# Performance work log

Measured on AMD Instinct MI355X. Metric: run time of the kernel, lower is better.

## Reference

```python
import jax, jax.numpy as jnp
import numpy as np

HIDDEN = 2048
NUM_EXPERTS = 64
TOP_K = 2


def setup_inputs() -> dict:
    key = jax.random.key(0)
    k1, k2 = jax.random.split(key)
    x = jax.random.normal(k1, (4, 4096, HIDDEN), dtype=jnp.float32)
    # nn.Linear(hidden, num_experts, bias=False): weight shape [E, H], y = x @ W.T
    W = jax.random.normal(k2, (NUM_EXPERTS, HIDDEN), dtype=jnp.float32) * (HIDDEN ** -0.5)
    return {"x": x, "W": W}


def reference(x, W):
    B, S, H = x.shape
    E, K = NUM_EXPERTS, TOP_K
    xf = x.reshape(-1, H)                       # [N, H]
    gate_logits = xf @ W.T                      # [N, E]
    routing_probs = jax.nn.softmax(gate_logits, axis=-1)
    top_k_probs, top_k_indices = jax.lax.top_k(routing_probs, K)  # [N, K]
    denom = jnp.sum(top_k_probs, axis=-1, keepdims=True) + 1e-6
    routing_weights = (top_k_probs / denom).reshape(B, S, K)
    expert_indices = top_k_indices.reshape(B, S, K)

    # aux load-balancing loss (training path)
    N = xf.shape[0]
    # expert_mask.mean(0): fraction of tokens assigned to each expert
    assign_per_expert = jnp.zeros((E,), jnp.float32).at[top_k_indices.reshape(-1)].add(1.0) / N
    prob_per_expert = jnp.mean(routing_probs, axis=0)             # [E]
    aux_loss = (jnp.sum(prob_per_expert * prob_per_expert) * E
                + jnp.sum(assign_per_expert * assign_per_expert) * E)

    # expert_counts update (bincount over selected indices)
    expert_counts = jnp.zeros((E,), jnp.float32).at[top_k_indices.reshape(-1)].add(1.0)

    return routing_weights, expert_indices, aux_loss, expert_counts
```

## Files before the change

kernel.cpp:

```cpp
#include <hip/hip_runtime.h>

#define HID 2048
#define NEXP 64
#define NTOK 16384
#define TM 32
#define NTHREADS 512
#define NCHUNK 32
#define KPH 8
#define CPW 4
#define TPW 4
#define WS_W_OFF 1024
#define CHUNK_B 24576

#define OUT_IDX_OFF (2 * NTOK)
#define OUT_AUX_OFF (4 * NTOK)
#define OUT_CNT_OFF (4 * NTOK + 1)

typedef __attribute__((ext_vector_type(8))) short bhalf8;
typedef __attribute__((ext_vector_type(16))) float f32x16;

__device__ __forceinline__ void split3(float v, unsigned short& h1, unsigned short& h2, unsigned short& h3) {
    unsigned int u = __float_as_uint(v);
    unsigned int r1 = (u + 0x7FFFu + ((u >> 16) & 1u)) & 0xFFFF0000u;
    float f1 = __uint_as_float(r1);
    float d1 = v - f1;
    unsigned int u2 = __float_as_uint(d1);
    unsigned int r2 = (u2 + 0x7FFFu + ((u2 >> 16) & 1u)) & 0xFFFF0000u;
    float f2 = __uint_as_float(r2);
    float d2 = d1 - f2;
    h1 = (unsigned short)(r1 >> 16);
    h2 = (unsigned short)(r2 >> 16);
    h3 = (unsigned short)(__float_as_uint(d2) >> 16);
}

__device__ __forceinline__ void xsplit(float4 va, float4 vb, bhalf8& o1, bhalf8& o2, bhalf8& o3) {
    float f[8] = {va.x, va.y, va.z, va.w, vb.x, vb.y, vb.z, vb.w};
    union U { bhalf8 v; unsigned int u[4]; } u1, u2, u3;
#pragma unroll
    for (int t = 0; t < 4; t++) {
        float a = f[2 * t], b = f[2 * t + 1];
        unsigned int ua = __float_as_uint(a), ub = __float_as_uint(b);
        float da = a - __uint_as_float(ua & 0xFFFF0000u);
        float db = b - __uint_as_float(ub & 0xFFFF0000u);
        unsigned int uda = __float_as_uint(da), udb = __float_as_uint(db);
        float da2 = da - __uint_as_float(uda & 0xFFFF0000u);
        float db2 = db - __uint_as_float(udb & 0xFFFF0000u);
        u1.u[t] = (ua >> 16) | (ub & 0xFFFF0000u);
        u2.u[t] = (uda >> 16) | (udb & 0xFFFF0000u);
        u3.u[t] = (__float_as_uint(da2) >> 16) | (__float_as_uint(db2) & 0xFFFF0000u);
    }
    o1 = u1.v; o2 = u2.v; o3 = u3.v;
}

__global__ __launch_bounds__(64) void wsplit_kernel(const float* __restrict__ W,
                                                    char* __restrict__ wq,
                                                    float* __restrict__ wsf) {
    if (blockIdx.x < 2) wsf[blockIdx.x * 64 + threadIdx.x] = 0.f;
    int idx8 = (blockIdx.x * 64 + threadIdx.x) * 8;
    int e = idx8 >> 11;
    int k0 = idx8 & 2047;
    int c = k0 >> 6, ks = (k0 >> 4) & 3, half = (k0 >> 3) & 1;
    int g = e >> 5, l = (e & 31) + 32 * half;
    const float4* wp = (const float4*)(W + (size_t)e * HID + k0);
    float4 v0 = wp[0], v1 = wp[1];
    float f[8] = {v0.x, v0.y, v0.z, v0.w, v1.x, v1.y, v1.z, v1.w};
    unsigned int p1[4], p2[4], p3[4];
#pragma unroll
    for (int t = 0; t < 4; t++) {
        unsigned short a1, a2, a3, b1, b2, b3;
        split3(f[2 * t], a1, a2, a3);
        split3(f[2 * t + 1], b1, b2, b3);
        p1[t] = (unsigned int)a1 | ((unsigned int)b1 << 16);
        p2[t] = (unsigned int)a2 | ((unsigned int)b2 << 16);
        p3[t] = (unsigned int)a3 | ((unsigned int)b3 << 16);
    }
    char* base = wq + (size_t)(((c * 4 + ks) * 3 + 0) * 2 + g) * 1024 + l * 16;
    *(uint4*)(base)        = make_uint4(p1[0], p1[1], p1[2], p1[3]);
    *(uint4*)(base + 2048) = make_uint4(p2[0], p2[1], p2[2], p2[3]);
    *(uint4*)(base + 4096) = make_uint4(p3[0], p3[1], p3[2], p3[3]);
}

__global__ __launch_bounds__(NTHREADS, 4) void router_main(
    const float* __restrict__ x, const char* __restrict__ wq,
    float* __restrict__ out, float* __restrict__ ws_accum)
{
    __shared__ float slab[KPH * TM * 68];
    __shared__ float scount[NEXP];
    __shared__ float sprob[NEXP];

    const int tid = threadIdx.x;
    const int w = tid >> 6;
    const int lane = tid & 63;
    const int r = lane & 31;
    const int h = lane >> 5;
    const int n0 = blockIdx.x * TM;

    const float* xrow = x + (size_t)(n0 + r) * HID + h * 8;

    f32x16 acc0, acc1;
#pragma unroll
    for (int i = 0; i < 16; i++) { acc0[i] = 0.f; acc1[i] = 0.f; }

#pragma unroll 1
    for (int i = 0; i < CPW; ++i) {
        const int c = w * CPW + i;
        const float* xc = xrow + c * 64;
        float4 pxa[4], pxb[4];
#pragma unroll
        for (int ks = 0; ks < 4; ks++) {
            pxa[ks] = *(const float4*)(xc + ks * 16);
            pxb[ks] = *(const float4*)(xc + ks * 16 + 4);
        }
        const char* wc = wq + (size_t)c * CHUNK_B + lane * 16;
#pragma unroll
        for (int ks = 0; ks < 4; ks++) {
            bhalf8 A1, A2, A3;
            xsplit(pxa[ks], pxb[ks], A1, A2, A3);
            const char* wk = wc + ks * 6144;
            bhalf8 B1 = *(const bhalf8*)(wk);
            bhalf8 B2 = *(const bhalf8*)(wk + 2048);
            bhalf8 B3 = *(const bhalf8*)(wk + 4096);
            bhalf8 C1 = *(const bhalf8*)(wk + 1024);
            bhalf8 C2 = *(const bhalf8*)(wk + 2048 + 1024);
            bhalf8 C3 = *(const bhalf8*)(wk + 4096 + 1024);
            acc0 = __builtin_amdgcn_mfma_f32_32x32x16_bf16(A1, B1, acc0, 0, 0, 0);
            acc0 = __builtin_amdgcn_mfma_f32_32x32x16_bf16(A1, B2, acc0, 0, 0, 0);
            acc0 = __builtin_amdgcn_mfma_f32_32x32x16_bf16(A2, B1, acc0, 0, 0, 0);
            acc0 = __builtin_amdgcn_mfma_f32_32x32x16_bf16(A1, B3, acc0, 0, 0, 0);
            acc0 = __builtin_amdgcn_mfma_f32_32x32x16_bf16(A2, B2, acc0, 0, 0, 0);
            acc0 = __builtin_amdgcn_mfma_f32_32x32x16_bf16(A3, B1, acc0, 0, 0, 0);
            acc1 = __builtin_amdgcn_mfma_f32_32x32x16_bf16(A1, C1, acc1, 0, 0, 0);
            acc1 = __builtin_amdgcn_mfma_f32_32x32x16_bf16(A1, C2, acc1, 0, 0, 0);
            acc1 = __builtin_amdgcn_mfma_f32_32x32x16_bf16(A2, C1, acc1, 0, 0, 0);
            acc1 = __builtin_amdgcn_mfma_f32_32x32x16_bf16(A1, C3, acc1, 0, 0, 0);
            acc1 = __builtin_amdgcn_mfma_f32_32x32x16_bf16(A2, C2, acc1, 0, 0, 0);
            acc1 = __builtin_amdgcn_mfma_f32_32x32x16_bf16(A3, C1, acc1, 0, 0, 0);
        }
    }

#pragma unroll
    for (int reg = 0; reg < 16; reg++) {
        int row = (reg & 3) + 8 * (reg >> 2) + 4 * h;
        slab[(w * TM + row) * 68 + r]      = acc0[reg];
        slab[(w * TM + row) * 68 + 32 + r] = acc1[reg];
    }
    if (tid < NEXP) { scount[tid] = 0.f; sprob[tid] = 0.f; }
    __syncthreads();

    float* logits = slab;
#pragma unroll
    for (int idx = tid; idx < TM * NEXP; idx += NTHREADS) {
        int t = idx >> 6, e = idx & 63;
        float v = 0.f;
#pragma unroll
        for (int p = 0; p < KPH; p++) v += slab[(p * TM + t) * 68 + e];
        logits[t * 68 + e] = v;
    }
    __syncthreads();

    float pacc = 0.f;
#pragma unroll 1
    for (int j = 0; j < TPW; j++) {
        const int t = w * TPW + j;
        const float v = logits[t * 68 + lane];
        float m1 = v, m2 = -3.4e38f;
        int i1 = lane, i2 = 0;
#pragma unroll
        for (int off = 32; off > 0; off >>= 1) {
            float om1 = __shfl_xor(m1, off);
            int   oi1 = __shfl_xor(i1, off);
            float om2 = __shfl_xor(m2, off);
            int   oi2 = __shfl_xor(i2, off);
            if (om1 > m1 || (om1 == m1 && oi1 < i1)) {
                if (m1 > om2 || (m1 == om2 && i1 < oi2)) { m2 = m1; i2 = i1; }
                else { m2 = om2; i2 = oi2; }
                m1 = om1; i1 = oi1;
            } else {
                if (om1 > m2 || (om1 == m2 && oi1 < i2)) { m2 = om1; i2 = oi1; }
            }
        }
        float p = __expf(v - m1);
        float Z = p;
#pragma unroll
        for (int off = 32; off > 0; off >>= 1) Z += __shfl_xor(Z, off);
        float invZ = 1.f / Z;
        pacc += p * invZ;
        if (lane == 0) {
            float p1 = invZ;
            float p2 = __expf(m2 - m1) * invZ;
            float denom = p1 + p2 + 1e-6f;
            int n = n0 + t;
            out[2 * n + 0] = p1 / denom;
            out[2 * n + 1] = p2 / denom;
            out[OUT_IDX_OFF + 2 * n + 0] = (float)i1;
            out[OUT_IDX_OFF + 2 * n + 1] = (float)i2;
            atomicAdd(&scount[i1], 1.f);
            atomicAdd(&scount[i2], 1.f);
        }
    }
    atomicAdd(&sprob[lane], pacc);
    __syncthreads();

    if (tid < NEXP) {
        atomicAdd(&ws_accum[tid], sprob[tid]);
        atomicAdd(&ws_accum[NEXP + tid], scount[tid]);
    }
}

__global__ void router_finish(const float* __restrict__ ws_accum,
                              float* __restrict__ out)
{
    const int e = threadIdx.x;
    const float invN = 1.f / (float)NTOK;
    float p = ws_accum[e] * invN;
    float a = ws_accum[NEXP + e] * invN;
    float v = p * p + a * a;
#pragma unroll
    for (int off = 32; off > 0; off >>= 1)
        v += __shfl_down(v, off);
    if (e == 0) out[OUT_AUX_OFF] = v * (float)NEXP;
    out[OUT_CNT_OFF + e] = ws_accum[NEXP + e];
}

extern "C" void kernel_launch(void* const* d_in, const int* in_sizes, int n_in,
                              void* d_out, int out_size, void* d_ws, size_t ws_size,
                              hipStream_t stream)
{
    const float* x = (const float*)d_in[0];
    const float* W = (const float*)d_in[1];
    float* out = (float*)d_out;
    float* wsf = (float*)d_ws;
    char* wq = (char*)d_ws + WS_W_OFF;

    wsplit_kernel<<<256, 64, 0, stream>>>(W, wq, wsf);
    router_main<<<NTOK / TM, NTHREADS, 0, stream>>>(x, wq, out, wsf);
    router_finish<<<1, 64, 0, stream>>>(wsf, out);
}
```

Before: 217.8 us.

## Fuse finish kernel via last-block counter and shrink logits slab with LDS atomics

```diff
diff --git a/kernel.cpp b/kernel.cpp
--- a/kernel.cpp
+++ b/kernel.cpp
@@ -5,10 +5,9 @@
 #define NTOK 16384
 #define TM 32
 #define NTHREADS 512
-#define NCHUNK 32
-#define KPH 8
 #define CPW 4
 #define TPW 4
+#define NBLK (NTOK / TM)
 #define WS_W_OFF 1024
 #define CHUNK_B 24576
 
@@ -55,7 +54,7 @@
 __global__ __launch_bounds__(64) void wsplit_kernel(const float* __restrict__ W,
                                                     char* __restrict__ wq,
                                                     float* __restrict__ wsf) {
-    if (blockIdx.x < 2) wsf[blockIdx.x * 64 + threadIdx.x] = 0.f;
+    if (blockIdx.x < 3) wsf[blockIdx.x * 64 + threadIdx.x] = 0.f;
     int idx8 = (blockIdx.x * 64 + threadIdx.x) * 8;
     int e = idx8 >> 11;
     int k0 = idx8 & 2047;
@@ -80,13 +79,16 @@
     *(uint4*)(base + 4096) = make_uint4(p3[0], p3[1], p3[2], p3[3]);
 }
 
-__global__ __launch_bounds__(NTHREADS, 4) void router_main(
+__global__ __launch_bounds__(NTHREADS)
+__attribute__((amdgpu_waves_per_eu(4, 4)))
+void router_main(
     const float* __restrict__ x, const char* __restrict__ wq,
-    float* __restrict__ out, float* __restrict__ ws_accum)
+    float* __restrict__ out, float* __restrict__ wsf)
 {
-    __shared__ float slab[KPH * TM * 68];
+    __shared__ float slab[TM * 68];
     __shared__ float scount[NEXP];
     __shared__ float sprob[NEXP];
+    __shared__ int slast;
 
     const int tid = threadIdx.x;
     const int w = tid >> 6;
@@ -94,6 +96,10 @@
     const int r = lane & 31;
     const int h = lane >> 5;
     const int n0 = blockIdx.x * TM;
+
+    for (int i = tid; i < TM * 68; i += NTHREADS) slab[i] = 0.f;
+    if (tid < NEXP) { scount[tid] = 0.f; sprob[tid] = 0.f; }
+    __syncthreads();
 
     const float* xrow = x + (size_t)(n0 + r) * HID + h * 8;
 
@@ -141,23 +147,12 @@
 #pragma unroll
     for (int reg = 0; reg < 16; reg++) {
         int row = (reg & 3) + 8 * (reg >> 2) + 4 * h;
-        slab[(w * TM + row) * 68 + r]      = acc0[reg];
-        slab[(w * TM + row) * 68 + 32 + r] = acc1[reg];
-    }
-    if (tid < NEXP) { scount[tid] = 0.f; sprob[tid] = 0.f; }
-    __syncthreads();
-
-    float* logits = slab;
-#pragma unroll
-    for (int idx = tid; idx < TM * NEXP; idx += NTHREADS) {
-        int t = idx >> 6, e = idx & 63;
-        float v = 0.f;
-#pragma unroll
-        for (int p = 0; p < KPH; p++) v += slab[(p * TM + t) * 68 + e];
-        logits[t * 68 + e] = v;
-    }
-    __syncthreads();
-
+        atomicAdd(&slab[row * 68 + r],      acc0[reg]);
+        atomicAdd(&slab[row * 68 + 32 + r], acc1[reg]);
+    }
+    __syncthreads();
+
+    const float* logits = slab;
     float pacc = 0.f;
 #pragma unroll 1
     for (int j = 0; j < TPW; j++) {
@@ -179,12 +174,12 @@
                 if (om1 > m2 || (om1 == m2 && oi1 < i2)) { m2 = om1; i2 = oi1; }
             }
         }
-        float p = __expf(v - m1);
-        float Z = p;
+        float pr = __expf(v - m1);
+        float Z = pr;
 #pragma unroll
         for (int off = 32; off > 0; off >>= 1) Z += __shfl_xor(Z, off);
         float invZ = 1.f / Z;
-        pacc += p * invZ;
+        pacc += pr * invZ;
         if (lane == 0) {
             float p1 = invZ;
             float p2 = __expf(m2 - m1) * invZ;
@@ -202,24 +197,31 @@
     __syncthreads();
 
     if (tid < NEXP) {
-        atomicAdd(&ws_accum[tid], sprob[tid]);
-        atomicAdd(&ws_accum[NEXP + tid], scount[tid]);
-    }
-}
-
-__global__ void router_finish(const float* __restrict__ ws_accum,
-                              float* __restrict__ out)
-{
-    const int e = threadIdx.x;
-    const float invN = 1.f / (float)NTOK;
-    float p = ws_accum[e] * invN;
-    float a = ws_accum[NEXP + e] * invN;
-    float v = p * p + a * a;
-#pragma unroll
-    for (int off = 32; off > 0; off >>= 1)
-        v += __shfl_down(v, off);
-    if (e == 0) out[OUT_AUX_OFF] = v * (float)NEXP;
-    out[OUT_CNT_OFF + e] = ws_accum[NEXP + e];
+        atomicAdd(&wsf[tid], sprob[tid]);
+        atomicAdd(&wsf[NEXP + tid], scount[tid]);
+    }
+
+    __threadfence();
+    if (tid == 0) {
+        unsigned prev = __hip_atomic_fetch_add((unsigned int*)(wsf + 2 * NEXP), 1u,
+                                               __ATOMIC_ACQ_REL, __HIP_MEMORY_SCOPE_AGENT);
+        slast = (prev == NBLK - 1) ? 1 : 0;
+    }
+    __syncthreads();
+    if (slast && tid < NEXP) {
+        const int e = tid;
+        const float invN = 1.f / (float)NTOK;
+        float ps = __hip_atomic_load(wsf + e, __ATOMIC_RELAXED, __HIP_MEMORY_SCOPE_AGENT);
+        float cs = __hip_atomic_load(wsf + NEXP + e, __ATOMIC_RELAXED, __HIP_MEMORY_SCOPE_AGENT);
+        out[OUT_CNT_OFF + e] = cs;
+        float pv = ps * invN;
+        float av = cs * invN;
+        float v = pv * pv + av * av;
+#pragma unroll
+        for (int off = 32; off > 0; off >>= 1)
+            v += __shfl_down(v, off);
+        if (e == 0) out[OUT_AUX_OFF] = v * (float)NEXP;
+    }
 }
 
 extern "C" void kernel_launch(void* const* d_in, const int* in_sizes, int n_in,
@@ -233,6 +235,5 @@
     char* wq = (char*)d_ws + WS_W_OFF;
 
     wsplit_kernel<<<256, 64, 0, stream>>>(W, wq, wsf);
-    router_main<<<NTOK / TM, NTHREADS, 0, stream>>>(x, wq, out, wsf);
-    router_finish<<<1, 64, 0, stream>>>(wsf, out);
-}
+    router_main<<<NBLK, NTHREADS, 0, stream>>>(x, wq, out, wsf);
+}
```

After: 301.0 us. 38.2% more time.
